# Kernel optimization log

Measured on AMD Instinct MI355X. Metric: run time of the kernel, lower is better.

The kernel has to match this reference:

```python
import jax, jax.numpy as jnp
import numpy as np

EXPERT_CAPACITY = 320
RMS_EPS = 1e-6


def setup_inputs() -> dict:
    key = jax.random.key(0)
    k1, k2, k3, k4 = jax.random.split(key, 4)
    B, S, D, E, F = 8, 2048, 1024, 8, 2048
    data = jax.random.normal(k1, (B, S, D), dtype=jnp.float32)
    gate_w = jax.random.normal(k2, (D, E), dtype=jnp.float32) * 0.02
    w1 = jax.random.normal(k3, (E, D, F), dtype=jnp.float32) * 0.02
    w2 = jax.random.normal(k4, (E, F, D), dtype=jnp.float32) * 0.02
    rms_w = jnp.ones((D,), dtype=jnp.float32)
    return {"data": data, "gate_w": gate_w, "w1": w1, "w2": w2, "rms_w": rms_w}


def reference(data, gate_w, w1, w2, rms_w):
    B, S, D = data.shape
    E = gate_w.shape[1]
    C = EXPERT_CAPACITY

    # norm_fn: RMSNorm
    var = jnp.mean(data * data, axis=-1, keepdims=True)
    norm = data * jax.lax.rsqrt(var + RMS_EPS) * rms_w  # [B,S,D]

    # route (fp32 gate, no jitter)
    logits = jnp.einsum('bsd,de->bse', norm, gate_w)  # [B,S,E]
    probs = jax.nn.softmax(logits, axis=-1)
    eidx = jnp.argmax(probs, axis=-1)  # [B,S] top-1 expert
    onehot = jax.nn.one_hot(eidx, E, dtype=jnp.int32)  # [B,S,E]
    priority = jnp.cumsum(onehot, axis=1)  # position within expert per batch row
    mask = onehot * (priority <= C)  # capacity-masked dispatch mask [B,S,E]

    pos = jnp.take_along_axis(priority, eidx[..., None], axis=2)[..., 0] - 1  # [B,S]
    kept = jnp.take_along_axis(mask, eidx[..., None], axis=2)[..., 0].astype(bool)
    pos_oob = jnp.where(kept, pos, C)  # OOB -> dropped on scatter

    # dispatch: scatter kept tokens into [B,E,C,D] buffers
    b_idx = jnp.arange(B)[:, None]  # broadcast over S
    buf = jnp.zeros((B, E, C, D), dtype=norm.dtype)
    buf = buf.at[b_idx, eidx, pos_oob].set(norm, mode='drop')

    # per-expert FFN with gelu_new (tanh approx)
    h = jax.nn.gelu(jnp.einsum('becd,edf->becf', buf, w1), approximate=True)
    out_buf = jnp.einsum('becf,efd->becd', h, w2)  # [B,E,C,D]

    # combine: gather expert output; dropped tokens keep norm_data (clone semantics)
    pos_c = jnp.clip(pos_oob, 0, C - 1)
    y = out_buf[b_idx, eidx, pos_c]  # [B,S,D]
    next_states = jnp.where(kept[..., None], y, norm)

    max_prob = jnp.max(probs, axis=-1, keepdims=True)
    hidden = max_prob * next_states
    final = data + hidden  # dropout rate 0

    expert_index_out = jnp.argmax(mask, axis=-1)  # matches torch argmax over masked one-hot
    return final, logits, expert_index_out
```

## Files before the change

### kernel.cpp

```cpp
#include <hip/hip_runtime.h>

typedef __attribute__((ext_vector_type(8))) __bf16 bf16x8;
typedef __attribute__((ext_vector_type(4))) float f32x4;

#define DEVI __device__ __forceinline__

DEVI unsigned short f2bf(float f) {
    unsigned u = __builtin_bit_cast(unsigned, f);
    u += 0x7fffu + ((u >> 16) & 1u);
    return (unsigned short)(u >> 16);
}
DEVI float bf2f(unsigned short h) {
    unsigned u = ((unsigned)h) << 16;
    return __builtin_bit_cast(float, u);
}
DEVI float gelu_tanh(float x) {
    float u = 0.7978845608028654f * (x + 0.044715f * x * x * x);
    float t = 1.0f - 2.0f / (1.0f + __expf(2.0f * u));
    return 0.5f * x * (1.0f + t);
}
DEVI void gload16(const void* g, void* l) {
    __builtin_amdgcn_global_load_lds((const __attribute__((address_space(1))) unsigned int*)g,
                                     (__attribute__((address_space(3))) unsigned int*)l,
                                     16, 0, 0);
}

#define BB 8
#define SS 2048
#define DD 1024
#define EE 8
#define FF 2048
#define CC 320
#define NTOK (BB * SS)
#define MPE (BB * CC)
#define NSLOT (EE * MPE)

__global__ __launch_bounds__(256) void k_rms_gate(
    const float* __restrict__ data, const float* __restrict__ gate_w,
    const float* __restrict__ rms_w, unsigned short* __restrict__ norm_bf,
    float* __restrict__ logits_out, float* __restrict__ maxprob, int* __restrict__ eidx_out)
{
    const int token = blockIdx.x;
    const int t = threadIdx.x;
    const float4 v = ((const float4*)(data + (size_t)token * DD))[t];
    float ss = v.x * v.x + v.y * v.y + v.z * v.z + v.w * v.w;
#pragma unroll
    for (int o = 32; o; o >>= 1) ss += __shfl_down(ss, o, 64);
    __shared__ float sred[4];
    __shared__ float slog[8];
    __shared__ float sacc[4][8];
    if ((t & 63) == 0) sred[t >> 6] = ss;
    __syncthreads();
    const float tot = sred[0] + sred[1] + sred[2] + sred[3];
    const float scale = rsqrtf(tot * (1.0f / 1024.0f) + 1e-6f);
    const float4 w = ((const float4*)rms_w)[t];
    float nn[4] = { v.x * scale * w.x, v.y * scale * w.y, v.z * scale * w.z, v.w * scale * w.w };
    ushort4 nb;
    nb.x = f2bf(nn[0]); nb.y = f2bf(nn[1]); nb.z = f2bf(nn[2]); nb.w = f2bf(nn[3]);
    ((ushort4*)(norm_bf + (size_t)token * DD))[t] = nb;

    float acc[8] = {0, 0, 0, 0, 0, 0, 0, 0};
    const float4* g = (const float4*)(gate_w + t * 32);
#pragma unroll
    for (int d = 0; d < 4; ++d) {
        float4 p = g[2 * d], q = g[2 * d + 1];
        acc[0] += nn[d] * p.x; acc[1] += nn[d] * p.y; acc[2] += nn[d] * p.z; acc[3] += nn[d] * p.w;
        acc[4] += nn[d] * q.x; acc[5] += nn[d] * q.y; acc[6] += nn[d] * q.z; acc[7] += nn[d] * q.w;
    }
#pragma unroll
    for (int e = 0; e < 8; ++e) {
#pragma unroll
        for (int o = 32; o; o >>= 1) acc[e] += __shfl_down(acc[e], o, 64);
    }
    if ((t & 63) == 0) {
#pragma unroll
        for (int e = 0; e < 8; ++e) sacc[t >> 6][e] = acc[e];
    }
    __syncthreads();
    if (t < 8) {
        float l = sacc[0][t] + sacc[1][t] + sacc[2][t] + sacc[3][t];
        logits_out[(size_t)token * 8 + t] = l;
        slog[t] = l;
    }
    __syncthreads();
    if (t == 0) {
        float m = slog[0]; int am = 0;
#pragma unroll
        for (int e = 1; e < 8; ++e) { if (slog[e] > m) { m = slog[e]; am = e; } }
        float s = 0.f;
#pragma unroll
        for (int e = 0; e < 8; ++e) s += __expf(slog[e] - m);
        maxprob[token] = 1.0f / s;
        eidx_out[token] = am;
    }
}

__global__ __launch_bounds__(256) void k_route(
    const int* __restrict__ eidx, int* __restrict__ pos_out,
    float* __restrict__ idxf_out, int* __restrict__ slot_token)
{
    const int b = blockIdx.x, t = threadIdx.x;
    for (int i = t; i < EE * CC; i += 256) {
        int e = i / CC, c = i % CC;
        slot_token[e * MPE + b * CC + c] = -1;
    }
    const int base = b * SS + t * 8;
    int e8[8];
#pragma unroll
    for (int j = 0; j < 8; ++j) e8[j] = eidx[base + j];
    int cnt[8] = {0, 0, 0, 0, 0, 0, 0, 0};
#pragma unroll
    for (int j = 0; j < 8; ++j) {
#pragma unroll
        for (int q = 0; q < 8; ++q) cnt[q] += (e8[j] == q);
    }
    __shared__ int sc[8][256];
#pragma unroll
    for (int q = 0; q < 8; ++q) sc[q][t] = cnt[q];
    __syncthreads();
    for (int off = 1; off < 256; off <<= 1) {
        int v[8];
#pragma unroll
        for (int q = 0; q < 8; ++q) v[q] = (t >= off) ? sc[q][t - off] : 0;
        __syncthreads();
#pragma unroll
        for (int q = 0; q < 8; ++q) sc[q][t] += v[q];
        __syncthreads();
    }
    int run[8];
#pragma unroll
    for (int q = 0; q < 8; ++q) run[q] = (t == 0) ? 0 : sc[q][t - 1];
#pragma unroll
    for (int j = 0; j < 8; ++j) {
        const int e = e8[j];
        const int tok = base + j;
        int pos = 0;
#pragma unroll
        for (int q = 0; q < 8; ++q) if (q == e) { pos = run[q]; run[q]++; }
        const bool kept = pos < CC;
        pos_out[tok] = kept ? pos : CC;
        idxf_out[tok] = (float)(kept ? e : 0);
        if (kept) slot_token[e * MPE + b * CC + pos] = tok;
    }
}

__global__ __launch_bounds__(256) void k_transcvt(
    const float* __restrict__ src, unsigned short* __restrict__ dst,
    int R, int C, int tiles_r, int tiles_c)
{
    const int bid = blockIdx.x;
    const int tpe = tiles_r * tiles_c;
    const int e = bid / tpe, rem = bid % tpe;
    const int tr = rem / tiles_c, tc = rem % tiles_c;
    __shared__ float tile[32][33];
    const int t = threadIdx.x, c = t & 31, r0 = t >> 5;
    const float* s = src + (size_t)e * R * C;
#pragma unroll
    for (int i = 0; i < 4; ++i) {
        int r = r0 + i * 8;
        tile[r][c] = s[(size_t)(tr * 32 + r) * C + tc * 32 + c];
    }
    __syncthreads();
    unsigned short* d = dst + (size_t)e * C * R;
#pragma unroll
    for (int i = 0; i < 4; ++i) {
        int r = r0 + i * 8;
        d[(size_t)(tc * 32 + r) * R + tr * 32 + c] = f2bf(tile[c][r]);
    }
}

__global__ __launch_bounds__(256) void k_gather(
    const unsigned short* __restrict__ norm_bf, const int* __restrict__ slot_token,
    unsigned short* __restrict__ Xbuf)
{
    const int slot = blockIdx.x;
    const int t = threadIdx.x;
    const int tok = slot_token[slot];
    ushort4* dst = (ushort4*)(Xbuf + (size_t)slot * DD);
    if (tok < 0) {
        ushort4 z; z.x = 0; z.y = 0; z.z = 0; z.w = 0;
        dst[t] = z;
    } else {
        dst[t] = ((const ushort4*)(norm_bf + (size_t)tok * DD))[t];
    }
}

template <int MODE>
__global__ __launch_bounds__(256) void k_gemm(
    const unsigned short* __restrict__ A, const unsigned short* __restrict__ Bt,
    unsigned short* __restrict__ H, const int* __restrict__ slot_token,
    const float* __restrict__ maxprob, const float* __restrict__ data,
    float* __restrict__ outF, int K, int N)
{
    const int ntn = N >> 7;
    const int tpe = 20 * ntn;
    const int bid = blockIdx.x;
    const int e = bid / tpe, rem = bid % tpe;
    const int tm = rem / ntn, tn = rem % ntn;

    __shared__ __align__(16) unsigned short sm[17408];
    unsigned short* lsA = sm;
    unsigned short* lsB = sm + 8192;

    const int tid = threadIdx.x;
    const int w = tid >> 6, L = tid & 63;
    const int wr = w >> 1, wc = w & 1;
    const int rr = L & 15, g = L >> 4;
    const int crow = L >> 3, csl = L & 7;
    const int ssl = csl ^ crow;

    const size_t Abase = ((size_t)e * MPE + (size_t)tm * 128) * (size_t)K;
    const size_t Bbase = ((size_t)e * N + (size_t)tn * 128) * (size_t)K;

    f32x4 acc[4][4];
#pragma unroll
    for (int m = 0; m < 4; ++m)
#pragma unroll
        for (int n = 0; n < 4; ++n) acc[m][n] = 0.f;

    const int KT = K >> 6;
    for (int kt = 0; kt < KT; ++kt) {
        const int k0 = kt << 6;
#pragma unroll
        for (int ch = 0; ch < 4; ++ch) {
            const int rowl = w * 32 + ch * 8 + crow;
            gload16(A + Abase + (size_t)rowl * K + (k0 + (ssl << 3)),
                    lsA + (w * 32 + ch * 8) * 64);
            gload16(Bt + Bbase + (size_t)rowl * K + (k0 + (ssl << 3)),
                    lsB + (w * 32 + ch * 8) * 64);
        }
        __syncthreads();
#pragma unroll
        for (int ks = 0; ks < 2; ++ks) {
            bf16x8 af[4], bfr[4];
#pragma unroll
            for (int m = 0; m < 4; ++m) {
                const int row = wr * 64 + m * 16 + rr;
                af[m] = *(const bf16x8*)(lsA + row * 64 + ((((ks << 2) | g) ^ (row & 7)) << 3));
            }
#pragma unroll
            for (int n = 0; n < 4; ++n) {
                const int row = wc * 64 + n * 16 + rr;
                bfr[n] = *(const bf16x8*)(lsB + row * 64 + ((((ks << 2) | g) ^ (row & 7)) << 3));
            }
#pragma unroll
            for (int m = 0; m < 4; ++m)
#pragma unroll
                for (int n = 0; n < 4; ++n)
                    acc[m][n] = __builtin_amdgcn_mfma_f32_16x16x32_bf16(af[m], bfr[n], acc[m][n], 0, 0, 0);
        }
        __syncthreads();
    }

    unsigned short* lo = sm;
#pragma unroll
    for (int m = 0; m < 4; ++m)
#pragma unroll
        for (int n = 0; n < 4; ++n) {
            f32x4 a = acc[m][n];
            const int rl = wr * 64 + m * 16 + g * 4;
            const int cl = wc * 64 + n * 16 + rr;
#pragma unroll
            for (int j = 0; j < 4; ++j) {
                float x = a[j];
                if (MODE == 0) x = gelu_tanh(x);
                lo[(rl + j) * 136 + cl] = f2bf(x);
            }
        }
    __syncthreads();

    if (MODE == 0) {
        const size_t hrow0 = (size_t)e * MPE + (size_t)tm * 128;
#pragma unroll
        for (int i = 0; i < 8; ++i) {
            const int ch2 = tid + i * 256;
            const int row = ch2 >> 4, off = (ch2 & 15) << 3;
            int4 vv = *(const int4*)(lo + row * 136 + off);
            *(int4*)(H + (hrow0 + row) * 2048 + tn * 128 + off) = vv;
        }
    } else {
        const int slot0 = e * MPE + tm * 128;
#pragma unroll
        for (int i = 0; i < 8; ++i) {
            const int ch2 = tid + i * 256;
            const int row = ch2 >> 4, off = (ch2 & 15) << 3;
            const int tok = slot_token[slot0 + row];
            if (tok < 0) continue;
            const float mp = maxprob[tok];
            int4 yv = *(const int4*)(lo + row * 136 + off);
            const unsigned short* yy = (const unsigned short*)&yv;
            const size_t go = (size_t)tok * DD + (size_t)(tn * 128 + off);
            float4 d0 = *(const float4*)(data + go);
            float4 d1 = *(const float4*)(data + go + 4);
            float4 o0, o1;
            o0.x = d0.x + mp * bf2f(yy[0]);
            o0.y = d0.y + mp * bf2f(yy[1]);
            o0.z = d0.z + mp * bf2f(yy[2]);
            o0.w = d0.w + mp * bf2f(yy[3]);
            o1.x = d1.x + mp * bf2f(yy[4]);
            o1.y = d1.y + mp * bf2f(yy[5]);
            o1.z = d1.z + mp * bf2f(yy[6]);
            o1.w = d1.w + mp * bf2f(yy[7]);
            *(float4*)(outF + go) = o0;
            *(float4*)(outF + go + 4) = o1;
        }
    }
}

__global__ __launch_bounds__(128) void k_fill(
    const int* __restrict__ pos, const float* __restrict__ maxprob,
    const unsigned short* __restrict__ norm_bf, const float* __restrict__ data,
    float* __restrict__ outF)
{
    const int tok = blockIdx.x;
    if (pos[tok] < CC) return;
    const float mp = maxprob[tok];
    const int t = threadIdx.x;
    const size_t o = (size_t)tok * DD + (size_t)t * 8;
    float4 d0 = *(const float4*)(data + o);
    float4 d1 = *(const float4*)(data + o + 4);
    ushort4 n0 = *(const ushort4*)(norm_bf + o);
    ushort4 n1 = *(const ushort4*)(norm_bf + o + 4);
    float4 r0, r1;
    r0.x = d0.x + mp * bf2f(n0.x);
    r0.y = d0.y + mp * bf2f(n0.y);
    r0.z = d0.z + mp * bf2f(n0.z);
    r0.w = d0.w + mp * bf2f(n0.w);
    r1.x = d1.x + mp * bf2f(n1.x);
    r1.y = d1.y + mp * bf2f(n1.y);
    r1.z = d1.z + mp * bf2f(n1.z);
    r1.w = d1.w + mp * bf2f(n1.w);
    *(float4*)(outF + o) = r0;
    *(float4*)(outF + o + 4) = r1;
}

extern "C" void kernel_launch(void* const* d_in, const int* in_sizes, int n_in,
                              void* d_out, int out_size, void* d_ws, size_t ws_size,
                              hipStream_t stream)
{
    (void)in_sizes; (void)n_in; (void)out_size; (void)ws_size;
    const float* data   = (const float*)d_in[0];
    const float* gate_w = (const float*)d_in[1];
    const float* w1     = (const float*)d_in[2];
    const float* w2     = (const float*)d_in[3];
    const float* rms_w  = (const float*)d_in[4];

    float* outF   = (float*)d_out;
    float* logits = outF + (size_t)NTOK * DD;
    float* idxf   = logits + (size_t)NTOK * EE;

    char* ws = (char*)d_ws;
    const size_t SZ_NORM = (size_t)NTOK * DD * 2;
    const size_t SZ_W1T  = (size_t)EE * DD * FF * 2;
    const size_t SZ_W2T  = SZ_W1T;
    const size_t SZ_X    = (size_t)NSLOT * DD * 2;
    const size_t SZ_H    = (size_t)NSLOT * FF * 2;
    unsigned short* norm_bf = (unsigned short*)(ws);
    unsigned short* w1T     = (unsigned short*)(ws + SZ_NORM);
    unsigned short* w2T     = (unsigned short*)(ws + SZ_NORM + SZ_W1T);
    unsigned short* Xbuf    = (unsigned short*)(ws + SZ_NORM + SZ_W1T + SZ_W2T);
    unsigned short* Hbuf    = (unsigned short*)(ws + SZ_NORM + SZ_W1T + SZ_W2T + SZ_X);
    char* small             = ws + SZ_NORM + SZ_W1T + SZ_W2T + SZ_X + SZ_H;
    int*   slot_token = (int*)(small);
    int*   pos        = (int*)(small + NSLOT * 4);
    int*   eidx       = (int*)(small + NSLOT * 4 + NTOK * 4);
    float* maxprob    = (float*)(small + NSLOT * 4 + NTOK * 4 + NTOK * 4);

    k_rms_gate<<<NTOK, 256, 0, stream>>>(data, gate_w, rms_w, norm_bf, logits, maxprob, eidx);
    k_route<<<BB, 256, 0, stream>>>(eidx, pos, idxf, slot_token);
    k_transcvt<<<EE * 32 * 64, 256, 0, stream>>>(w1, w1T, DD, FF, 32, 64);
    k_transcvt<<<EE * 64 * 32, 256, 0, stream>>>(w2, w2T, FF, DD, 64, 32);
    k_gather<<<NSLOT, 256, 0, stream>>>(norm_bf, slot_token, Xbuf);
    k_gemm<0><<<EE * 20 * (FF / 128), 256, 0, stream>>>(Xbuf, w1T, Hbuf, nullptr, nullptr, nullptr, nullptr, DD, FF);
    k_gemm<1><<<EE * 20 * (DD / 128), 256, 0, stream>>>(Hbuf, w2T, nullptr, slot_token, maxprob, data, outF, FF, DD);
    k_fill<<<NTOK, 128, 0, stream>>>(pos, maxprob, norm_bf, data, outF);
}
```

Baseline: 544.4 us.

## Fuse token gather into first expert GEMM and merge weight transpose launches

The first expert GEMM now loads A rows straight from the normalized token buffer through per-row pointers taken from slot_token, with empty slots pointing at a zeroed page. This removes the separate gather kernel and the Xbuf write and re-read. The two weight transpose/convert launches are merged into one grid, and the GEMM block index is reordered so that expert is the fastest-varying dimension. The zero page (512 ints, 2 KB) covers one full K=1024 bf16 row, but the indirect loads may coalesce less well than contiguous Xbuf rows.

```diff
diff --git a/kernel.cpp b/kernel.cpp
--- a/kernel.cpp
+++ b/kernel.cpp
@@ -97,9 +97,12 @@
 
 __global__ __launch_bounds__(256) void k_route(
     const int* __restrict__ eidx, int* __restrict__ pos_out,
-    float* __restrict__ idxf_out, int* __restrict__ slot_token)
+    float* __restrict__ idxf_out, int* __restrict__ slot_token, int* __restrict__ zp)
 {
     const int b = blockIdx.x, t = threadIdx.x;
+    if (b == 0) {
+        zp[t] = 0; zp[t + 256] = 0;
+    }
     for (int i = t; i < EE * CC; i += 256) {
         int e = i / CC, c = i % CC;
         slot_token[e * MPE + b * CC + c] = -1;
@@ -144,16 +147,11 @@
     }
 }
 
-__global__ __launch_bounds__(256) void k_transcvt(
-    const float* __restrict__ src, unsigned short* __restrict__ dst,
-    int R, int C, int tiles_r, int tiles_c)
-{
-    const int bid = blockIdx.x;
-    const int tpe = tiles_r * tiles_c;
-    const int e = bid / tpe, rem = bid % tpe;
-    const int tr = rem / tiles_c, tc = rem % tiles_c;
+DEVI void transcvt_tile(const float* __restrict__ src, unsigned short* __restrict__ dst,
+                        int R, int C, int e, int tr, int tc, int t)
+{
     __shared__ float tile[32][33];
-    const int t = threadIdx.x, c = t & 31, r0 = t >> 5;
+    const int c = t & 31, r0 = t >> 5;
     const float* s = src + (size_t)e * R * C;
 #pragma unroll
     for (int i = 0; i < 4; ++i) {
@@ -169,19 +167,19 @@
     }
 }
 
-__global__ __launch_bounds__(256) void k_gather(
-    const unsigned short* __restrict__ norm_bf, const int* __restrict__ slot_token,
-    unsigned short* __restrict__ Xbuf)
-{
-    const int slot = blockIdx.x;
+__global__ __launch_bounds__(256) void k_transcvt2(
+    const float* __restrict__ w1, const float* __restrict__ w2,
+    unsigned short* __restrict__ w1T, unsigned short* __restrict__ w2T)
+{
+    const int bid = blockIdx.x;
     const int t = threadIdx.x;
-    const int tok = slot_token[slot];
-    ushort4* dst = (ushort4*)(Xbuf + (size_t)slot * DD);
-    if (tok < 0) {
-        ushort4 z; z.x = 0; z.y = 0; z.z = 0; z.w = 0;
-        dst[t] = z;
+    if (bid < EE * 32 * 64) {
+        const int e = bid / (32 * 64), rem = bid % (32 * 64);
+        transcvt_tile(w1, w1T, DD, FF, e, rem / 64, rem % 64, t);
     } else {
-        dst[t] = ((const ushort4*)(norm_bf + (size_t)tok * DD))[t];
+        const int b2 = bid - EE * 32 * 64;
+        const int e = b2 / (64 * 32), rem = b2 % (64 * 32);
+        transcvt_tile(w2, w2T, FF, DD, e, rem / 32, rem % 32, t);
     }
 }
 
@@ -190,13 +188,13 @@
     const unsigned short* __restrict__ A, const unsigned short* __restrict__ Bt,
     unsigned short* __restrict__ H, const int* __restrict__ slot_token,
     const float* __restrict__ maxprob, const float* __restrict__ data,
-    float* __restrict__ outF, int K, int N)
+    float* __restrict__ outF, const unsigned short* __restrict__ zp, int K, int N)
 {
     const int ntn = N >> 7;
-    const int tpe = 20 * ntn;
     const int bid = blockIdx.x;
-    const int e = bid / tpe, rem = bid % tpe;
-    const int tm = rem / ntn, tn = rem % ntn;
+    const int e = bid & 7;
+    const int inner = bid >> 3;
+    const int tm = inner / ntn, tn = inner % ntn;
 
     __shared__ __align__(16) unsigned short sm[17408];
     unsigned short* lsA = sm;
@@ -209,8 +207,22 @@
     const int crow = L >> 3, csl = L & 7;
     const int ssl = csl ^ crow;
 
-    const size_t Abase = ((size_t)e * MPE + (size_t)tm * 128) * (size_t)K;
+    const int slot0 = e * MPE + tm * 128;
     const size_t Bbase = ((size_t)e * N + (size_t)tn * 128) * (size_t)K;
+
+    const unsigned short* aptr[4];
+    const unsigned short* bptr[4];
+#pragma unroll
+    for (int ch = 0; ch < 4; ++ch) {
+        const int rowl = w * 32 + ch * 8 + crow;
+        if (MODE == 0) {
+            const int tok = slot_token[slot0 + rowl];
+            aptr[ch] = (tok < 0) ? zp : (A + (size_t)tok * DD);
+        } else {
+            aptr[ch] = A + ((size_t)slot0 + rowl) * (size_t)K;
+        }
+        bptr[ch] = Bt + Bbase + (size_t)rowl * K;
+    }
 
     f32x4 acc[4][4];
 #pragma unroll
@@ -220,14 +232,11 @@
 
     const int KT = K >> 6;
     for (int kt = 0; kt < KT; ++kt) {
-        const int k0 = kt << 6;
+        const int koff = (kt << 6) + (ssl << 3);
 #pragma unroll
         for (int ch = 0; ch < 4; ++ch) {
-            const int rowl = w * 32 + ch * 8 + crow;
-            gload16(A + Abase + (size_t)rowl * K + (k0 + (ssl << 3)),
-                    lsA + (w * 32 + ch * 8) * 64);
-            gload16(Bt + Bbase + (size_t)rowl * K + (k0 + (ssl << 3)),
-                    lsB + (w * 32 + ch * 8) * 64);
+            gload16(aptr[ch] + koff, lsA + (w * 32 + ch * 8) * 64);
+            gload16(bptr[ch] + koff, lsB + (w * 32 + ch * 8) * 64);
         }
         __syncthreads();
 #pragma unroll
@@ -270,7 +279,7 @@
     __syncthreads();
 
     if (MODE == 0) {
-        const size_t hrow0 = (size_t)e * MPE + (size_t)tm * 128;
+        const size_t hrow0 = (size_t)slot0;
 #pragma unroll
         for (int i = 0; i < 8; ++i) {
             const int ch2 = tid + i * 256;
@@ -279,7 +288,6 @@
             *(int4*)(H + (hrow0 + row) * 2048 + tn * 128 + off) = vv;
         }
     } else {
-        const int slot0 = e * MPE + tm * 128;
 #pragma unroll
         for (int i = 0; i < 8; ++i) {
             const int ch2 = tid + i * 256;
@@ -353,25 +361,22 @@
     const size_t SZ_NORM = (size_t)NTOK * DD * 2;
     const size_t SZ_W1T  = (size_t)EE * DD * FF * 2;
     const size_t SZ_W2T  = SZ_W1T;
-    const size_t SZ_X    = (size_t)NSLOT * DD * 2;
     const size_t SZ_H    = (size_t)NSLOT * FF * 2;
     unsigned short* norm_bf = (unsigned short*)(ws);
     unsigned short* w1T     = (unsigned short*)(ws + SZ_NORM);
     unsigned short* w2T     = (unsigned short*)(ws + SZ_NORM + SZ_W1T);
-    unsigned short* Xbuf    = (unsigned short*)(ws + SZ_NORM + SZ_W1T + SZ_W2T);
-    unsigned short* Hbuf    = (unsigned short*)(ws + SZ_NORM + SZ_W1T + SZ_W2T + SZ_X);
-    char* small             = ws + SZ_NORM + SZ_W1T + SZ_W2T + SZ_X + SZ_H;
+    unsigned short* Hbuf    = (unsigned short*)(ws + SZ_NORM + SZ_W1T + SZ_W2T);
+    char* small             = ws + SZ_NORM + SZ_W1T + SZ_W2T + SZ_H;
     int*   slot_token = (int*)(small);
     int*   pos        = (int*)(small + NSLOT * 4);
     int*   eidx       = (int*)(small + NSLOT * 4 + NTOK * 4);
     float* maxprob    = (float*)(small + NSLOT * 4 + NTOK * 4 + NTOK * 4);
+    int*   zp         = (int*)(small + NSLOT * 4 + NTOK * 4 + NTOK * 4 + NTOK * 4);
 
     k_rms_gate<<<NTOK, 256, 0, stream>>>(data, gate_w, rms_w, norm_bf, logits, maxprob, eidx);
-    k_route<<<BB, 256, 0, stream>>>(eidx, pos, idxf, slot_token);
-    k_transcvt<<<EE * 32 * 64, 256, 0, stream>>>(w1, w1T, DD, FF, 32, 64);
-    k_transcvt<<<EE * 64 * 32, 256, 0, stream>>>(w2, w2T, FF, DD, 64, 32);
-    k_gather<<<NSLOT, 256, 0, stream>>>(norm_bf, slot_token, Xbuf);
-    k_gemm<0><<<EE * 20 * (FF / 128), 256, 0, stream>>>(Xbuf, w1T, Hbuf, nullptr, nullptr, nullptr, nullptr, DD, FF);
-    k_gemm<1><<<EE * 20 * (DD / 128), 256, 0, stream>>>(Hbuf, w2T, nullptr, slot_token, maxprob, data, outF, FF, DD);
+    k_route<<<BB, 256, 0, stream>>>(eidx, pos, idxf, slot_token, zp);
+    k_transcvt2<<<EE * 32 * 64 * 2, 256, 0, stream>>>(w1, w2, w1T, w2T);
+    k_gemm<0><<<EE * 20 * (FF / 128), 256, 0, stream>>>(norm_bf, w1T, Hbuf, slot_token, nullptr, nullptr, nullptr, (const unsigned short*)zp, DD, FF);
+    k_gemm<1><<<EE * 20 * (DD / 128), 256, 0, stream>>>(Hbuf, w2T, nullptr, slot_token, maxprob, data, outF, nullptr, FF, DD);
     k_fill<<<NTOK, 128, 0, stream>>>(pos, maxprob, norm_bf, data, outF);
 }
```

New measurement: 522.0 us. 4.1% less time.
